# Kernel tuning notes

Measured on AMD Instinct MI355X. Metric: run time of the kernel, lower is better.

The kernel has to match this reference:

```python
import jax, jax.numpy as jnp
import numpy as np

B, N, C, OUT = 4, 512, 128, 128

def setup_inputs() -> dict:
    key = jax.random.key(0)
    k1, k2, k3 = jax.random.split(key, 3)
    adj_matrix = jax.random.bernoulli(k1, 0.1, (B, N, N)).astype(jnp.float32)
    features = jax.random.normal(k2, (B, N, C), dtype=jnp.float32)
    # xavier_uniform for Linear(2C -> OUT): weight stored here as [2C, OUT]
    limit = float(np.sqrt(6.0 / (2 * C + OUT)))
    W = jax.random.uniform(k3, (2 * C, OUT), minval=-limit, maxval=limit, dtype=jnp.float32)
    b = jnp.zeros((OUT,), dtype=jnp.float32)
    return {"adj_matrix": adj_matrix, "features": features, "W": W, "b": b}

def reference(adj_matrix, features, W, b):
    # pooling aggregator: masked max over neighbors (materializes [B,N,N,C], as in source)
    neg_inf = jnp.finfo(features.dtype).min
    mask = (adj_matrix > 0)[..., None]                      # [B,N,N,1]
    feat_nb = jnp.where(mask, features[:, None, :, :], neg_inf)  # [B,N,N,C]
    agg = jnp.max(feat_nb, axis=2)                          # [B,N,C]
    agg = jnp.where(jnp.isfinite(agg), agg, 0.0)
    neigh = jax.nn.relu(agg)
    combined = jnp.concatenate([features, neigh], axis=-1)  # [B,N,2C]
    return jnp.einsum('bnc,co->bno', combined, W) + b       # [B,N,OUT]
```

## Files before the change

### kernel.cpp

```cpp
#include <hip/hip_runtime.h>
#include <hip/hip_bf16.h>
#include <float.h>


#define Bsz 4
#define Nn  512
#define Cc  128
#define OUTn 128
#define NNODES (Bsz * Nn)
#define KK (2 * Cc)

typedef __bf16 bf16x8 __attribute__((ext_vector_type(8)));
typedef float  f32x4  __attribute__((ext_vector_type(4)));

static __device__ __forceinline__ unsigned short f2bf(float x) {
    __hip_bfloat16 h = __float2bfloat16(x);
    return *reinterpret_cast<unsigned short*>(&h);
}
static __device__ __forceinline__ __bf16 f2bf16(float x) {
    unsigned short u = f2bf(x);
    return *reinterpret_cast<__bf16*>(&u);
}

__global__ __launch_bounds__(256) void sage_agg(
    const float* __restrict__ adj,
    const float* __restrict__ feat,
    unsigned short* __restrict__ comb)
{
    const int w = threadIdx.x >> 6;
    const int l = threadIdx.x & 63;
    const int node = blockIdx.x;
    const int b = node >> 9;
    const int i = node & (Nn - 1);

    __shared__ unsigned short nbr[4][128];
    __shared__ float2 pmax[4][64];

    const float* adjrow = adj + (size_t)node * Nn;
    const float2* f2 = (const float2*)(feat + (size_t)b * Nn * Cc);

    int cnt = 0;
    #pragma unroll
    for (int ch = 0; ch < 2; ++ch) {
        int j = w * 128 + ch * 64 + l;
        float a = adjrow[j];
        unsigned long long mask = __ballot(a > 0.0f);
        int pos = __popcll(mask & ((1ull << l) - 1ull));
        if (a > 0.0f) nbr[w][cnt + pos] = (unsigned short)j;
        cnt += __popcll(mask);
    }

    float m0 = -FLT_MAX, m1 = -FLT_MAX;
    int k = 0;
    for (; k + 4 <= cnt; k += 4) {
        int j0 = nbr[w][k + 0], j1 = nbr[w][k + 1];
        int j2 = nbr[w][k + 2], j3 = nbr[w][k + 3];
        float2 v0 = f2[j0 * 64 + l];
        float2 v1 = f2[j1 * 64 + l];
        float2 v2 = f2[j2 * 64 + l];
        float2 v3 = f2[j3 * 64 + l];
        m0 = fmaxf(m0, fmaxf(fmaxf(v0.x, v1.x), fmaxf(v2.x, v3.x)));
        m1 = fmaxf(m1, fmaxf(fmaxf(v0.y, v1.y), fmaxf(v2.y, v3.y)));
    }
    for (; k < cnt; ++k) {
        int j = nbr[w][k];
        float2 v = f2[j * 64 + l];
        m0 = fmaxf(m0, v.x);
        m1 = fmaxf(m1, v.y);
    }
    pmax[w][l] = make_float2(m0, m1);
    __syncthreads();

    if (w == 0) {
        float2 p0 = pmax[0][l], p1 = pmax[1][l], p2 = pmax[2][l], p3 = pmax[3][l];
        float n0 = fmaxf(fmaxf(p0.x, p1.x), fmaxf(p2.x, p3.x));
        float n1 = fmaxf(fmaxf(p0.y, p1.y), fmaxf(p2.y, p3.y));
        n0 = fmaxf(n0, 0.0f);
        n1 = fmaxf(n1, 0.0f);
        float2 s = f2[i * 64 + l];

        ushort2* crow = (ushort2*)(comb + (size_t)node * KK);
        ushort2 sv; sv.x = f2bf(s.x); sv.y = f2bf(s.y);
        ushort2 nv; nv.x = f2bf(n0);  nv.y = f2bf(n1);
        crow[l]      = sv;
        crow[64 + l] = nv;
    }
}

__global__ __launch_bounds__(256) void sage_gemm(
    const __bf16* __restrict__ A,
    const float* __restrict__ W,
    const float* __restrict__ bias,
    float* __restrict__ out)
{
    const int wave = threadIdx.x >> 6;
    const int lane = threadIdx.x & 63;
    const int tile = blockIdx.x * 4 + wave;
    const int nt = tile & 7;
    const int mt = tile >> 3;

    const int frow = lane & 15;
    const int koff = (lane >> 4) * 8;

    const __bf16* pa = A + (size_t)(mt * 16 + frow) * KK + koff;
    const float*  wp = W + nt * 16 + frow;

    f32x4 acc = {0.f, 0.f, 0.f, 0.f};
    #pragma unroll
    for (int ks = 0; ks < KK / 32; ++ks) {
        bf16x8 af = *(const bf16x8*)(pa + ks * 32);
        bf16x8 bf;
        #pragma unroll
        for (int j = 0; j < 8; ++j) {
            bf[j] = f2bf16(wp[(size_t)(ks * 32 + koff + j) * OUTn]);
        }
        acc = __builtin_amdgcn_mfma_f32_16x16x32_bf16(af, bf, acc, 0, 0, 0);
    }

    const int col = lane & 15;
    const int r0  = (lane >> 4) * 4;
    const float bv = bias[nt * 16 + col];
    #pragma unroll
    for (int r = 0; r < 4; ++r) {
        out[(size_t)(mt * 16 + r0 + r) * OUTn + nt * 16 + col] = acc[r] + bv;
    }
}

extern "C" void kernel_launch(void* const* d_in, const int* in_sizes, int n_in,
                              void* d_out, int out_size, void* d_ws, size_t ws_size,
                              hipStream_t stream) {
    const float* adj  = (const float*)d_in[0];
    const float* feat = (const float*)d_in[1];
    const float* W    = (const float*)d_in[2];
    const float* bias = (const float*)d_in[3];
    float* out = (float*)d_out;

    unsigned short* comb = (unsigned short*)d_ws;

    sage_agg <<<dim3(NNODES), dim3(256), 0, stream>>>(adj, feat, comb);
    sage_gemm<<<dim3(NNODES / 16 * (OUTn / 16) / 4), dim3(256), 0, stream>>>(
        (const __bf16*)comb, W, bias, out);
}
```

Baseline: 68.53 us.

## Fuse neighbor max aggregation and GEMM into one kernel via shared memory

Merges the aggregation and GEMM kernels into a single launch. Each 512-thread block handles 8 nodes, one wave per node scanning the full adjacency row. The bf16 combined rows stay in LDS, zero-padded to 16 rows for the MFMA, and each wave then computes one 16-column output tile. This removes the global round-trip of the intermediate and one launch, but only 256 blocks run, each wave walks all ~51 neighbors serially instead of splitting across four waves, and half of each MFMA is wasted on padding rows.

```diff
diff --git a/kernel.cpp b/kernel.cpp
--- a/kernel.cpp
+++ b/kernel.cpp
@@ -9,6 +9,7 @@
 #define OUTn 128
 #define NNODES (Bsz * Nn)
 #define KK (2 * Cc)
+#define ROWP 264
 
 typedef __bf16 bf16x8 __attribute__((ext_vector_type(8)));
 typedef float  f32x4  __attribute__((ext_vector_type(4)));
@@ -22,27 +23,34 @@
     return *reinterpret_cast<__bf16*>(&u);
 }
 
-__global__ __launch_bounds__(256) void sage_agg(
+__global__ __launch_bounds__(512) void sage_fused(
     const float* __restrict__ adj,
     const float* __restrict__ feat,
-    unsigned short* __restrict__ comb)
+    const float* __restrict__ W,
+    const float* __restrict__ bias,
+    float* __restrict__ out)
 {
     const int w = threadIdx.x >> 6;
     const int l = threadIdx.x & 63;
-    const int node = blockIdx.x;
+    const int node = blockIdx.x * 8 + w;
     const int b = node >> 9;
     const int i = node & (Nn - 1);
 
-    __shared__ unsigned short nbr[4][128];
-    __shared__ float2 pmax[4][64];
+    __shared__ unsigned short nbr[8][Nn];
+    __shared__ unsigned short s_comb[16][ROWP];
+
+    {
+        unsigned int* z = (unsigned int*)&s_comb[8][0];
+        for (int idx = threadIdx.x; idx < 8 * ROWP / 2; idx += 512) z[idx] = 0u;
+    }
 
     const float* adjrow = adj + (size_t)node * Nn;
     const float2* f2 = (const float2*)(feat + (size_t)b * Nn * Cc);
 
     int cnt = 0;
     #pragma unroll
-    for (int ch = 0; ch < 2; ++ch) {
-        int j = w * 128 + ch * 64 + l;
+    for (int ch = 0; ch < Nn / 64; ++ch) {
+        int j = ch * 64 + l;
         float a = adjrow[j];
         unsigned long long mask = __ballot(a > 0.0f);
         int pos = __popcll(mask & ((1ull << l) - 1ull));
@@ -68,61 +76,45 @@
         m0 = fmaxf(m0, v.x);
         m1 = fmaxf(m1, v.y);
     }
-    pmax[w][l] = make_float2(m0, m1);
-    __syncthreads();
 
-    if (w == 0) {
-        float2 p0 = pmax[0][l], p1 = pmax[1][l], p2 = pmax[2][l], p3 = pmax[3][l];
-        float n0 = fmaxf(fmaxf(p0.x, p1.x), fmaxf(p2.x, p3.x));
-        float n1 = fmaxf(fmaxf(p0.y, p1.y), fmaxf(p2.y, p3.y));
-        n0 = fmaxf(n0, 0.0f);
-        n1 = fmaxf(n1, 0.0f);
-        float2 s = f2[i * 64 + l];
+    float n0 = fmaxf(m0, 0.0f), n1 = fmaxf(m1, 0.0f);
+    float2 s = f2[i * 64 + l];
 
-        ushort2* crow = (ushort2*)(comb + (size_t)node * KK);
+    {
+        ushort2* crow = (ushort2*)&s_comb[w][0];
         ushort2 sv; sv.x = f2bf(s.x); sv.y = f2bf(s.y);
         ushort2 nv; nv.x = f2bf(n0);  nv.y = f2bf(n1);
         crow[l]      = sv;
         crow[64 + l] = nv;
     }
-}
+    __syncthreads();
 
-__global__ __launch_bounds__(256) void sage_gemm(
-    const __bf16* __restrict__ A,
-    const float* __restrict__ W,
-    const float* __restrict__ bias,
-    float* __restrict__ out)
-{
-    const int wave = threadIdx.x >> 6;
-    const int lane = threadIdx.x & 63;
-    const int tile = blockIdx.x * 4 + wave;
-    const int nt = tile & 7;
-    const int mt = tile >> 3;
-
-    const int frow = lane & 15;
-    const int koff = (lane >> 4) * 8;
-
-    const __bf16* pa = A + (size_t)(mt * 16 + frow) * KK + koff;
-    const float*  wp = W + nt * 16 + frow;
+    const int nt = w;
+    const int frow = l & 15;
+    const int koff = (l >> 4) * 8;
+    const float* wp = W + nt * 16 + frow;
 
     f32x4 acc = {0.f, 0.f, 0.f, 0.f};
     #pragma unroll
     for (int ks = 0; ks < KK / 32; ++ks) {
-        bf16x8 af = *(const bf16x8*)(pa + ks * 32);
-        bf16x8 bf;
+        bf16x8 af = *(const bf16x8*)&s_comb[frow][ks * 32 + koff];
+        bf16x8 bfr;
         #pragma unroll
         for (int j = 0; j < 8; ++j) {
-            bf[j] = f2bf16(wp[(size_t)(ks * 32 + koff + j) * OUTn]);
+            bfr[j] = f2bf16(wp[(size_t)(ks * 32 + koff + j) * OUTn]);
         }
-        acc = __builtin_amdgcn_mfma_f32_16x16x32_bf16(af, bf, acc, 0, 0, 0);
+        acc = __builtin_amdgcn_mfma_f32_16x16x32_bf16(af, bfr, acc, 0, 0, 0);
     }
 
-    const int col = lane & 15;
-    const int r0  = (lane >> 4) * 4;
+    const int col = l & 15;
+    const int r0  = (l >> 4) * 4;
     const float bv = bias[nt * 16 + col];
     #pragma unroll
     for (int r = 0; r < 4; ++r) {
-        out[(size_t)(mt * 16 + r0 + r) * OUTn + nt * 16 + col] = acc[r] + bv;
+        int row = r0 + r;
+        if (row < 8) {
+            out[(size_t)(blockIdx.x * 8 + row) * OUTn + nt * 16 + col] = acc[r] + bv;
+        }
     }
 }
 
@@ -135,9 +127,5 @@
     const float* bias = (const float*)d_in[3];
     float* out = (float*)d_out;
 
-    unsigned short* comb = (unsigned short*)d_ws;
-
-    sage_agg <<<dim3(NNODES), dim3(256), 0, stream>>>(adj, feat, comb);
-    sage_gemm<<<dim3(NNODES / 16 * (OUTn / 16) / 4), dim3(256), 0, stream>>>(
-        (const __bf16*)comb, W, bias, out);
+    sage_fused<<<dim3(NNODES / 8), dim3(512), 0, stream>>>(adj, feat, W, bias, out);
 }
```

Measured after the change: 69.74 us. About the same (+1.8%).

## Fuse aggregation and linear projection into one per-node kernel with fp32 GEMV

Applied to the files above, without the earlier changes.

Merges the max-pool aggregation kernel and the MFMA bf16 GEMM into a single kernel. Each block now computes its node's combined vector in shared memory and does an fp32 GEMV against W, split across two halves of K, then adds bias. This removes a launch and the intermediate bf16 round-trip through the workspace. In exchange every block rereads the full 128 KB W from cache, and the projection runs on scalar FMAs instead of matrix cores.

```diff
diff --git a/kernel.cpp b/kernel.cpp
--- a/kernel.cpp
+++ b/kernel.cpp
@@ -10,22 +10,12 @@
 #define NNODES (Bsz * Nn)
 #define KK (2 * Cc)
 
-typedef __bf16 bf16x8 __attribute__((ext_vector_type(8)));
-typedef float  f32x4  __attribute__((ext_vector_type(4)));
-
-static __device__ __forceinline__ unsigned short f2bf(float x) {
-    __hip_bfloat16 h = __float2bfloat16(x);
-    return *reinterpret_cast<unsigned short*>(&h);
-}
-static __device__ __forceinline__ __bf16 f2bf16(float x) {
-    unsigned short u = f2bf(x);
-    return *reinterpret_cast<__bf16*>(&u);
-}
-
-__global__ __launch_bounds__(256) void sage_agg(
+__global__ __launch_bounds__(256) void sage_fused(
     const float* __restrict__ adj,
     const float* __restrict__ feat,
-    unsigned short* __restrict__ comb)
+    const float* __restrict__ W,
+    const float* __restrict__ bias,
+    float* __restrict__ out)
 {
     const int w = threadIdx.x >> 6;
     const int l = threadIdx.x & 63;
@@ -35,6 +25,8 @@
 
     __shared__ unsigned short nbr[4][128];
     __shared__ float2 pmax[4][64];
+    __shared__ float  s_comb[KK];
+    __shared__ float  s_part[2][OUTn];
 
     const float* adjrow = adj + (size_t)node * Nn;
     const float2* f2 = (const float2*)(feat + (size_t)b * Nn * Cc);
@@ -78,51 +70,25 @@
         n0 = fmaxf(n0, 0.0f);
         n1 = fmaxf(n1, 0.0f);
         float2 s = f2[i * 64 + l];
+        ((float2*)s_comb)[l]      = s;
+        ((float2*)s_comb)[64 + l] = make_float2(n0, n1);
+    }
+    __syncthreads();
 
-        ushort2* crow = (ushort2*)(comb + (size_t)node * KK);
-        ushort2 sv; sv.x = f2bf(s.x); sv.y = f2bf(s.y);
-        ushort2 nv; nv.x = f2bf(n0);  nv.y = f2bf(n1);
-        crow[l]      = sv;
-        crow[64 + l] = nv;
+    const int n = threadIdx.x & (OUTn - 1);
+    const int h = threadIdx.x >> 7;
+    const float* wp = W + (size_t)h * 128 * OUTn + n;
+
+    float acc = 0.0f;
+    #pragma unroll 8
+    for (int kk = 0; kk < 128; ++kk) {
+        acc = fmaf(s_comb[h * 128 + kk], wp[(size_t)kk * OUTn], acc);
     }
-}
+    s_part[h][n] = acc;
+    __syncthreads();
 
-__global__ __launch_bounds__(256) void sage_gemm(
-    const __bf16* __restrict__ A,
-    const float* __restrict__ W,
-    const float* __restrict__ bias,
-    float* __restrict__ out)
-{
-    const int wave = threadIdx.x >> 6;
-    const int lane = threadIdx.x & 63;
-    const int tile = blockIdx.x * 4 + wave;
-    const int nt = tile & 7;
-    const int mt = tile >> 3;
-
-    const int frow = lane & 15;
-    const int koff = (lane >> 4) * 8;
-
-    const __bf16* pa = A + (size_t)(mt * 16 + frow) * KK + koff;
-    const float*  wp = W + nt * 16 + frow;
-
-    f32x4 acc = {0.f, 0.f, 0.f, 0.f};
-    #pragma unroll
-    for (int ks = 0; ks < KK / 32; ++ks) {
-        bf16x8 af = *(const bf16x8*)(pa + ks * 32);
-        bf16x8 bf;
-        #pragma unroll
-        for (int j = 0; j < 8; ++j) {
-            bf[j] = f2bf16(wp[(size_t)(ks * 32 + koff + j) * OUTn]);
-        }
-        acc = __builtin_amdgcn_mfma_f32_16x16x32_bf16(af, bf, acc, 0, 0, 0);
-    }
-
-    const int col = lane & 15;
-    const int r0  = (lane >> 4) * 4;
-    const float bv = bias[nt * 16 + col];
-    #pragma unroll
-    for (int r = 0; r < 4; ++r) {
-        out[(size_t)(mt * 16 + r0 + r) * OUTn + nt * 16 + col] = acc[r] + bv;
+    if (threadIdx.x < OUTn) {
+        out[(size_t)node * OUTn + n] = s_part[0][n] + s_part[1][n] + bias[n];
     }
 }
 
@@ -135,9 +101,5 @@
     const float* bias = (const float*)d_in[3];
     float* out = (float*)d_out;
 
-    unsigned short* comb = (unsigned short*)d_ws;
-
-    sage_agg <<<dim3(NNODES), dim3(256), 0, stream>>>(adj, feat, comb);
-    sage_gemm<<<dim3(NNODES / 16 * (OUTn / 16) / 4), dim3(256), 0, stream>>>(
-        (const __bf16*)comb, W, bias, out);
+    sage_fused<<<dim3(NNODES), dim3(256), 0, stream>>>(adj, feat, W, bias, out);
 }
```

Result: slower. 72.27 us (+5.5%).
